# Kernel tuning notes

Hardware: AMD Instinct MI355X
Metric: run time of the kernel (lower is better)

Reference implementation:

```python
import jax, jax.numpy as jnp
import numpy as np

L, B, E, H, NL = 512, 8, 1024, 16, 2
HD = E // H
DFF = 4 * E
EPS = 1e-5


def setup_inputs() -> dict:
    key = jax.random.key(0)
    ks = jax.random.split(key, 8)
    s = 0.02
    return {
        "src": jax.random.normal(ks[0], (L, B, E), jnp.float32),
        "position_embed": jax.random.normal(ks[1], (L, L, HD), jnp.float32) * s,
        "type_embed": jax.random.normal(ks[2], (L, L, HD), jnp.float32) * s,
        "Wi": jax.random.normal(ks[3], (NL, 3 * E, E), jnp.float32) * s,
        "bi": jnp.zeros((NL, 3 * E), jnp.float32),
        "Wo": jax.random.normal(ks[4], (NL, E, E), jnp.float32) * s,
        "bo": jnp.zeros((NL, E), jnp.float32),
        "W1": jax.random.normal(ks[5], (NL, DFF, E), jnp.float32) * s,
        "b1": jnp.zeros((NL, DFF), jnp.float32),
        "W2": jax.random.normal(ks[6], (NL, E, DFF), jnp.float32) * s,
        "b2": jnp.zeros((NL, E), jnp.float32),
        "g1": jnp.ones((NL, E), jnp.float32),
        "be1": jnp.zeros((NL, E), jnp.float32),
        "g2": jnp.ones((NL, E), jnp.float32),
        "be2": jnp.zeros((NL, E), jnp.float32),
    }


def _ln(x, g, b):
    m = jnp.mean(x, -1, keepdims=True)
    v = jnp.mean((x - m) ** 2, -1, keepdims=True)
    return (x - m) * jax.lax.rsqrt(v + EPS) * g + b


def _attn(src, pos, typ, Wi, bi, Wo, bo):
    # src: [L, B, E]
    p = src @ Wi.T + bi                      # [L, B, 3E]
    q, k, v = jnp.split(p, 3, axis=-1)
    q = q * (HD ** -0.5)
    # -> [B, H, L, HD]
    def hsplit(t):
        return t.reshape(L, B, H, HD).transpose(1, 2, 0, 3)
    q, k, v = hsplit(q), hsplit(k), hsplit(v)
    # scores = q k^T + type_embed@q + q@pos^T  (Shaw relative attention)
    scores = jnp.einsum('bhld,bhsd->bhls', q, k)
    scores = scores + jnp.einsum('bhld,lsd->bhls', q, pos)      # position term
    scores = scores + jnp.einsum('lsd,bhld->bhls', typ, q)      # type term
    w = jax.nn.softmax(scores, axis=-1)                          # [B, H, L, S]
    # output = w v + w@pos + typ^T@w
    out = jnp.einsum('bhls,bhsd->bhld', w, v)
    out = out + jnp.einsum('bhls,lsd->bhld', w, pos)
    out = out + jnp.einsum('bhls,lsd->bhld', w, typ)
    out = out.transpose(2, 0, 1, 3).reshape(L, B, E)            # [L, B, E]
    return out @ Wo.T + bo


def _layer(src, pos, typ, Wi, bi, Wo, bo, W1, b1, W2, b2, g1, be1, g2, be2):
    src2 = _attn(src, pos, typ, Wi, bi, Wo, bo)
    src = _ln(src + src2, g1, be1)
    h = jax.nn.gelu(src @ W1.T + b1, approximate=False)
    src2 = h @ W2.T + b2
    return _ln(src + src2, g2, be2)


def reference(src, position_embed, type_embed, Wi, bi, Wo, bo, W1, b1, W2, b2,
              g1, be1, g2, be2):
    out = src
    for i in range(NL):
        out = _layer(out, position_embed, type_embed,
                     Wi[i], bi[i], Wo[i], bo[i], W1[i], b1[i], W2[i], b2[i],
                     g1[i], be1[i], g2[i], be2[i])
    return out
```

## Files before the change

kernel.cpp:

```cpp
#include <hip/hip_runtime.h>
#include <hip/hip_bf16.h>
#include <math.h>


typedef __hip_bfloat16 bf16;
typedef short short8 __attribute__((ext_vector_type(8)));
typedef float f32x4 __attribute__((ext_vector_type(4)));

constexpr int Lc = 512;
constexpr int Bc = 8;
constexpr int Ec = 1024;
constexpr int Hc = 16;
constexpr int HDc = 64;
constexpr int NLc = 2;
constexpr int DFFc = 4096;
constexpr int LB = Lc * Bc;
constexpr int BHc = Bc * Hc;
constexpr float EPSc = 1e-5f;

__device__ inline unsigned short f2bfu(float f) {
  union { __hip_bfloat16 h; unsigned short u; } cv;
  cv.h = __float2bfloat16(f);
  return cv.u;
}

template <bool ACC, bool GELU, bool OBF>
__global__ __launch_bounds__(256) void gemm_bt(
    int M, int N, int K,
    const bf16* __restrict__ A, int lda, long long sAz,
    const bf16* __restrict__ Bm, int ldb, long long sBz,
    void* __restrict__ Cv, int ldc, long long sCz,
    const float* __restrict__ bias) {
  __shared__ __align__(16) bf16 As[128 * 72];
  __shared__ __align__(16) bf16 Bs[64 * 72];
  const int tid = threadIdx.x;
  const int w = tid >> 6, lane = tid & 63, quad = lane >> 4, lr = lane & 15;
  const int m0 = blockIdx.x * 128, n0 = blockIdx.y * 64;
  const long long z = blockIdx.z;
  A += z * sAz;
  Bm += z * sBz;
  float* Cf = (float*)Cv;
  bf16* Cb = (bf16*)Cv;

  f32x4 acc[2][4];
#pragma unroll
  for (int i = 0; i < 2; i++)
#pragma unroll
    for (int j = 0; j < 4; j++) acc[i][j] = {0.f, 0.f, 0.f, 0.f};

  for (int k0 = 0; k0 < K; k0 += 64) {
#pragma unroll
    for (int i = 0; i < 8; i++) {
      int slot = tid + i * 256;
      int r = slot >> 4, c4 = (slot & 15) << 2;
      const bf16* srcp = A + (long long)(m0 + r) * lda + k0 + c4;
      *(ushort4*)&As[r * 72 + c4] = *(const ushort4*)srcp;
    }
#pragma unroll
    for (int i = 0; i < 4; i++) {
      int slot = tid + i * 256;
      int r = slot >> 4, c4 = (slot & 15) << 2;
      const bf16* srcp = Bm + (long long)(n0 + r) * ldb + k0 + c4;
      *(ushort4*)&Bs[r * 72 + c4] = *(const ushort4*)srcp;
    }
    __syncthreads();
#pragma unroll
    for (int ks = 0; ks < 64; ks += 32) {
      short8 a[2], b[4];
#pragma unroll
      for (int i = 0; i < 2; i++)
        a[i] = *(const short8*)&As[(w * 32 + i * 16 + lr) * 72 + ks + quad * 8];
#pragma unroll
      for (int j = 0; j < 4; j++)
        b[j] = *(const short8*)&Bs[(j * 16 + lr) * 72 + ks + quad * 8];
#pragma unroll
      for (int i = 0; i < 2; i++)
#pragma unroll
        for (int j = 0; j < 4; j++)
          acc[i][j] = __builtin_amdgcn_mfma_f32_16x16x32_bf16(a[i], b[j], acc[i][j], 0, 0, 0);
    }
    __syncthreads();
  }

#pragma unroll
  for (int i = 0; i < 2; i++) {
#pragma unroll
    for (int j = 0; j < 4; j++) {
      int col = n0 + j * 16 + lr;
      float bv = bias ? bias[col] : 0.f;
#pragma unroll
      for (int r = 0; r < 4; r++) {
        int row = m0 + w * 32 + i * 16 + quad * 4 + r;
        long long off = z * sCz + (long long)row * ldc + col;
        float v = acc[i][j][r] + bv;
        if (ACC) v += Cf[off];
        if (GELU) v = 0.5f * v * (1.f + erff(v * 0.70710678118654752f));
        if (OBF)
          Cb[off] = __float2bfloat16(v);
        else
          Cf[off] = v;
      }
    }
  }
}

__global__ void cvt_bf16(const float* __restrict__ in, bf16* __restrict__ out, long long n) {
  long long i = (long long)blockIdx.x * 256 + threadIdx.x;
  if (i < n) out[i] = __float2bfloat16(in[i]);
}

__global__ void init_x(const float* __restrict__ src, float* __restrict__ x, bf16* __restrict__ xb) {
  long long i = (long long)blockIdx.x * 256 + threadIdx.x;
  float v = src[i];
  x[i] = v;
  xb[i] = __float2bfloat16(v);
}

__global__ void prep_R(const float* __restrict__ pos, const float* __restrict__ typ,
                       bf16* __restrict__ Rb, bf16* __restrict__ Rt) {
  __shared__ __align__(16) float Ls[64 * 68];
  int l = blockIdx.y, s0 = blockIdx.x * 64;
  int tid = threadIdx.x;
#pragma unroll
  for (int i = 0; i < 4; i++) {
    int slot = tid + i * 256;
    int r = slot >> 4, c = (slot & 15) << 2;
    long long off = (((long long)l) * Lc + s0 + r) * HDc + c;
    float4 a = *(const float4*)&pos[off];
    float4 b = *(const float4*)&typ[off];
    float4 s = {a.x + b.x, a.y + b.y, a.z + b.z, a.w + b.w};
    *(float4*)&Ls[r * 68 + c] = s;
    ushort4 o = {f2bfu(s.x), f2bfu(s.y), f2bfu(s.z), f2bfu(s.w)};
    *(ushort4*)&Rb[off] = o;
  }
  __syncthreads();
#pragma unroll
  for (int i = 0; i < 4; i++) {
    int slot = tid + i * 256;
    int d = slot >> 4, s4 = (slot & 15) << 2;
    ushort4 o = {f2bfu(Ls[(s4 + 0) * 68 + d]), f2bfu(Ls[(s4 + 1) * 68 + d]),
                 f2bfu(Ls[(s4 + 2) * 68 + d]), f2bfu(Ls[(s4 + 3) * 68 + d])};
    *(ushort4*)&Rt[(((long long)l) * HDc + d) * Lc + s0 + s4] = o;
  }
}

__global__ void split_qk(const float* __restrict__ P, bf16* __restrict__ q, bf16* __restrict__ k) {
  long long idx = (long long)blockIdx.x * 256 + threadIdx.x;
  int col = idx & (Ec - 1);
  long long row = idx >> 10;
  int l = (int)(row >> 3), b = (int)(row & 7);
  int h = col >> 6, d = col & 63;
  long long dst = (((long long)(b * Hc + h)) * Lc + l) * HDc + d;
  q[dst] = __float2bfloat16(P[row * 3072 + col] * 0.125f);
  k[dst] = __float2bfloat16(P[row * 3072 + Ec + col]);
}

__global__ void transpose_v(const float* __restrict__ P, bf16* __restrict__ vt) {
  __shared__ __align__(16) float Ls[64 * 68];
  int bh = blockIdx.y, b = bh >> 4, h = bh & 15;
  int l0 = blockIdx.x * 64;
  int tid = threadIdx.x;
#pragma unroll
  for (int i = 0; i < 4; i++) {
    int slot = tid + i * 256;
    int r = slot >> 4, c = (slot & 15) << 2;
    float4 v = *(const float4*)&P[((long long)(l0 + r) * Bc + b) * 3072 + 2 * Ec + h * 64 + c];
    *(float4*)&Ls[r * 68 + c] = v;
  }
  __syncthreads();
#pragma unroll
  for (int i = 0; i < 4; i++) {
    int slot = tid + i * 256;
    int d = slot >> 4, s4 = (slot & 15) << 2;
    ushort4 o = {f2bfu(Ls[(s4 + 0) * 68 + d]), f2bfu(Ls[(s4 + 1) * 68 + d]),
                 f2bfu(Ls[(s4 + 2) * 68 + d]), f2bfu(Ls[(s4 + 3) * 68 + d])};
    *(ushort4*)&vt[(((long long)(b * Hc + h)) * HDc + d) * Lc + l0 + s4] = o;
  }
}

__global__ __launch_bounds__(256) void softmax_rows(const float* S, bf16* P) {
  int w = threadIdx.x >> 6, lane = threadIdx.x & 63;
  long long row = (long long)blockIdx.x * 4 + w;
  const float* sr = S + row * 512;
  float4 v0 = *(const float4*)(sr + lane * 4);
  float4 v1 = *(const float4*)(sr + 256 + lane * 4);
  float mx = fmaxf(fmaxf(fmaxf(v0.x, v0.y), fmaxf(v0.z, v0.w)),
                   fmaxf(fmaxf(v1.x, v1.y), fmaxf(v1.z, v1.w)));
#pragma unroll
  for (int o = 32; o; o >>= 1) mx = fmaxf(mx, __shfl_xor(mx, o, 64));
  float e[8];
  e[0] = __expf(v0.x - mx); e[1] = __expf(v0.y - mx);
  e[2] = __expf(v0.z - mx); e[3] = __expf(v0.w - mx);
  e[4] = __expf(v1.x - mx); e[5] = __expf(v1.y - mx);
  e[6] = __expf(v1.z - mx); e[7] = __expf(v1.w - mx);
  float sum = e[0] + e[1] + e[2] + e[3] + e[4] + e[5] + e[6] + e[7];
#pragma unroll
  for (int o = 32; o; o >>= 1) sum += __shfl_xor(sum, o, 64);
  float inv = 1.f / sum;
  ushort4 o0 = {f2bfu(e[0] * inv), f2bfu(e[1] * inv), f2bfu(e[2] * inv), f2bfu(e[3] * inv)};
  ushort4 o1 = {f2bfu(e[4] * inv), f2bfu(e[5] * inv), f2bfu(e[6] * inv), f2bfu(e[7] * inv)};
  *(ushort4*)(P + row * 1024 + lane * 4) = o0;
  *(ushort4*)(P + row * 1024 + 256 + lane * 4) = o1;
}

__global__ void merge_ao(const float* __restrict__ ao2, bf16* __restrict__ aob) {
  long long i = (long long)blockIdx.x * 256 + threadIdx.x;
  int d = (int)(i & 63);
  long long t = i >> 6;
  int l = (int)(t & (Lc - 1));
  long long bh = t >> 9;
  int b = (int)(bh >> 4), h = (int)(bh & 15);
  aob[((long long)(l * Bc + b)) * Ec + h * 64 + d] = __float2bfloat16(ao2[i]);
}

__global__ __launch_bounds__(256) void add_ln(const float* __restrict__ X, const float* __restrict__ Cin,
                                              const float* __restrict__ g, const float* __restrict__ be,
                                              float* __restrict__ outF, bf16* __restrict__ outB) {
  __shared__ float s_sum[4], s_sq[4];
  long long row = blockIdx.x;
  int tid = threadIdx.x;
  float4 xv = *(const float4*)&X[row * Ec + tid * 4];
  float4 cv = *(const float4*)&Cin[row * Ec + tid * 4];
  float v[4] = {xv.x + cv.x, xv.y + cv.y, xv.z + cv.z, xv.w + cv.w};
  float sm = v[0] + v[1] + v[2] + v[3];
  float sq = v[0] * v[0] + v[1] * v[1] + v[2] * v[2] + v[3] * v[3];
#pragma unroll
  for (int o = 32; o; o >>= 1) {
    sm += __shfl_xor(sm, o, 64);
    sq += __shfl_xor(sq, o, 64);
  }
  int w = tid >> 6, lane = tid & 63;
  if (lane == 0) {
    s_sum[w] = sm;
    s_sq[w] = sq;
  }
  __syncthreads();
  sm = s_sum[0] + s_sum[1] + s_sum[2] + s_sum[3];
  sq = s_sq[0] + s_sq[1] + s_sq[2] + s_sq[3];
  float mean = sm * (1.f / Ec);
  float var = sq * (1.f / Ec) - mean * mean;
  float rs = rsqrtf(var + EPSc);
#pragma unroll
  for (int e = 0; e < 4; e++) {
    int n = tid * 4 + e;
    float o = (v[e] - mean) * rs * g[n] + be[n];
    outF[row * Ec + n] = o;
    outB[row * Ec + n] = __float2bfloat16(o);
  }
}

static constexpr size_t WS_NEED = 327155712;

struct GlobalWs {
  void* p = nullptr;
  GlobalWs() {
    if (hipMalloc(&p, WS_NEED) != hipSuccess) p = nullptr;
  }
};
static GlobalWs g_ws;

extern "C" void kernel_launch(void* const* d_in, const int* in_sizes, int n_in,
                              void* d_out, int out_size, void* d_ws, size_t ws_size,
                              hipStream_t stream) {
  const float* src = (const float*)d_in[0];
  const float* pos = (const float*)d_in[1];
  const float* typ = (const float*)d_in[2];
  const float* Wi = (const float*)d_in[3];
  const float* bi = (const float*)d_in[4];
  const float* Wo = (const float*)d_in[5];
  const float* bo = (const float*)d_in[6];
  const float* W1 = (const float*)d_in[7];
  const float* b1 = (const float*)d_in[8];
  const float* W2 = (const float*)d_in[9];
  const float* b2 = (const float*)d_in[10];
  const float* g1 = (const float*)d_in[11];
  const float* be1 = (const float*)d_in[12];
  const float* g2 = (const float*)d_in[13];
  const float* be2 = (const float*)d_in[14];
  float* out = (float*)d_out;
  (void)in_sizes; (void)n_in; (void)out_size;

  char* wp = (ws_size >= WS_NEED) ? (char*)d_ws : (char*)g_ws.p;
  if (!wp) wp = (char*)d_ws;
  auto alloc = [&](size_t bytes) {
    char* r = wp;
    wp += (bytes + 255) & ~(size_t)255;
    return r;
  };

  char* U = alloc((size_t)BHc * Lc * Lc * 4);
  float* P = (float*)U;
  float* scores = (float*)U;
  bf16* probs = (bf16*)U;
  bf16* hb = (bf16*)U;

  float* x = (float*)alloc((size_t)LB * Ec * 4);
  bf16* xb = (bf16*)alloc((size_t)LB * Ec * 2);
  bf16* q = (bf16*)alloc((size_t)BHc * Lc * HDc * 2);
  bf16* k = (bf16*)alloc((size_t)BHc * Lc * HDc * 2);
  bf16* vt = (bf16*)alloc((size_t)BHc * HDc * Lc * 2);
  float* ao2 = (float*)alloc((size_t)BHc * Lc * HDc * 4);
  float* c1 = ao2;
  bf16* aob = (bf16*)alloc((size_t)LB * Ec * 2);
  bf16* Rb = (bf16*)alloc((size_t)Lc * Lc * HDc * 2);
  bf16* Rt = (bf16*)alloc((size_t)Lc * HDc * Lc * 2);
  bf16* wib = (bf16*)alloc((size_t)NLc * 3 * Ec * Ec * 2);
  bf16* wob = (bf16*)alloc((size_t)NLc * Ec * Ec * 2);
  bf16* w1b = (bf16*)alloc((size_t)NLc * DFFc * Ec * 2);
  bf16* w2b = (bf16*)alloc((size_t)NLc * Ec * DFFc * 2);

  {
    long long n;
    n = (long long)NLc * 3 * Ec * Ec;
    cvt_bf16<<<(int)((n + 255) / 256), 256, 0, stream>>>(Wi, wib, n);
    n = (long long)NLc * Ec * Ec;
    cvt_bf16<<<(int)((n + 255) / 256), 256, 0, stream>>>(Wo, wob, n);
    n = (long long)NLc * DFFc * Ec;
    cvt_bf16<<<(int)((n + 255) / 256), 256, 0, stream>>>(W1, w1b, n);
    n = (long long)NLc * Ec * DFFc;
    cvt_bf16<<<(int)((n + 255) / 256), 256, 0, stream>>>(W2, w2b, n);
  }
  prep_R<<<dim3(Lc / 64, Lc), 256, 0, stream>>>(pos, typ, Rb, Rt);
  init_x<<<LB * Ec / 256, 256, 0, stream>>>(src, x, xb);

  for (int i = 0; i < NLc; i++) {
    const bf16* Wi_b = wib + (size_t)i * 3 * Ec * Ec;
    const bf16* Wo_b = wob + (size_t)i * Ec * Ec;
    const bf16* W1_b = w1b + (size_t)i * DFFc * Ec;
    const bf16* W2_b = w2b + (size_t)i * Ec * DFFc;

    gemm_bt<false, false, false><<<dim3(LB / 128, 3 * Ec / 64, 1), 256, 0, stream>>>(
        LB, 3 * Ec, Ec, xb, Ec, 0, Wi_b, Ec, 0, P, 3 * Ec, 0, bi + (size_t)i * 3 * Ec);
    split_qk<<<LB * Ec / 256, 256, 0, stream>>>(P, q, k);
    transpose_v<<<dim3(Lc / 64, BHc), 256, 0, stream>>>(P, vt);

    gemm_bt<false, false, false><<<dim3(Lc / 128, Lc / 64, BHc), 256, 0, stream>>>(
        Lc, Lc, HDc, q, HDc, (long long)Lc * HDc, k, HDc, (long long)Lc * HDc,
        scores, Lc, (long long)Lc * Lc, nullptr);
    gemm_bt<true, false, false><<<dim3(1, Lc / 64, Lc), 256, 0, stream>>>(
        BHc, Lc, HDc, q, Lc * HDc, (long long)HDc, Rb, HDc, (long long)Lc * HDc,
        scores, Lc * Lc, (long long)Lc, nullptr);

    softmax_rows<<<BHc * Lc / 4, 256, 0, stream>>>(scores, probs);

    gemm_bt<false, false, false><<<dim3(Lc / 128, 1, BHc), 256, 0, stream>>>(
        Lc, HDc, Lc, probs, 1024, (long long)Lc * 1024, vt, Lc, (long long)HDc * Lc,
        ao2, HDc, (long long)Lc * HDc, nullptr);
    gemm_bt<true, false, false><<<dim3(1, 1, Lc), 256, 0, stream>>>(
        BHc, HDc, Lc, probs, Lc * 1024, (long long)1024, Rt, Lc, (long long)HDc * Lc,
        ao2, Lc * HDc, (long long)HDc, nullptr);

    merge_ao<<<BHc * Lc * HDc / 256, 256, 0, stream>>>(ao2, aob);

    gemm_bt<false, false, false><<<dim3(LB / 128, Ec / 64, 1), 256, 0, stream>>>(
        LB, Ec, Ec, aob, Ec, 0, Wo_b, Ec, 0, c1, Ec, 0, bo + (size_t)i * Ec);
    add_ln<<<LB, 256, 0, stream>>>(x, c1, g1 + (size_t)i * Ec, be1 + (size_t)i * Ec, x, xb);

    gemm_bt<false, true, true><<<dim3(LB / 128, DFFc / 64, 1), 256, 0, stream>>>(
        LB, DFFc, Ec, xb, Ec, 0, W1_b, Ec, 0, hb, DFFc, 0, b1 + (size_t)i * DFFc);
    gemm_bt<false, false, false><<<dim3(LB / 128, Ec / 64, 1), 256, 0, stream>>>(
        LB, Ec, DFFc, hb, DFFc, 0, W2_b, DFFc, 0, c1, Ec, 0, b2 + (size_t)i * Ec);

    float* outF = (i == NLc - 1) ? out : x;
    add_ln<<<LB, 256, 0, stream>>>(x, c1, g2 + (size_t)i * Ec, be2 + (size_t)i * Ec, outF, xb);
  }
}
```

Baseline: 1.221 ms.

## Add 128x128 GEMM with direct-to-LDS async loads and XOR swizzle

Adds a new GEMM kernel with a 128x128 output tile (4x4 MFMA tiles per wave in a 2x2 wave grid) that loads A/B tiles via global_load_lds directly into LDS using an XOR-swizzled layout instead of padded rows. The projection, FFN and QK/position-score GEMMs now use it, doubling reuse per loaded tile and avoiding register staging and padding. It uses more accumulator registers and halves the block count in the N dimension, which may reduce occupancy. The kernel has no double buffering, so loads still serialize with compute.

```diff
diff --git a/kernel.cpp b/kernel.cpp
--- a/kernel.cpp
+++ b/kernel.cpp
@@ -22,6 +22,100 @@
   union { __hip_bfloat16 h; unsigned short u; } cv;
   cv.h = __float2bfloat16(f);
   return cv.u;
+}
+
+__device__ inline void async16(const bf16* gsrc, bf16* ldst) {
+  __builtin_amdgcn_global_load_lds(
+      (const __attribute__((address_space(1))) void*)gsrc,
+      (__attribute__((address_space(3))) void*)ldst, 16, 0, 0);
+}
+
+template <bool ACC, bool GELU, bool OBF>
+__global__ __launch_bounds__(256) void gemm128(
+    int M, int N, int K,
+    const bf16* __restrict__ A, long long lda, long long sAz,
+    const bf16* __restrict__ Bm, long long ldb, long long sBz,
+    void* __restrict__ Cv, long long ldc, long long sCz,
+    const float* __restrict__ bias) {
+  __shared__ __align__(16) bf16 As[128 * 64];
+  __shared__ __align__(16) bf16 Bs[128 * 64];
+  const int tid = threadIdx.x;
+  const int w = tid >> 6, lane = tid & 63, quad = lane >> 4, lr = lane & 15;
+  const int wm = w >> 1, wn = w & 1;
+  const int m0 = blockIdx.x * 128, n0 = blockIdx.y * 128;
+  const long long z = blockIdx.z;
+  const bf16* Az = A + z * sAz;
+  const bf16* Bz = Bm + z * sBz;
+  float* Cf = (float*)Cv;
+  bf16* Cb = (bf16*)Cv;
+
+  const int srow = lane >> 3, sj = lane & 7;
+  const int sc = sj ^ srow;
+
+  f32x4 acc[4][4];
+#pragma unroll
+  for (int i = 0; i < 4; i++)
+#pragma unroll
+    for (int j = 0; j < 4; j++) acc[i][j] = {0.f, 0.f, 0.f, 0.f};
+
+  for (int k0 = 0; k0 < K; k0 += 64) {
+#pragma unroll
+    for (int s = 0; s < 4; s++) {
+      int li = w * 4 + s;
+      int r = li * 8 + srow;
+      async16(Az + (long long)(m0 + r) * lda + k0 + sc * 8, &As[li * 512]);
+    }
+#pragma unroll
+    for (int s = 0; s < 4; s++) {
+      int li = w * 4 + s;
+      int r = li * 8 + srow;
+      async16(Bz + (long long)(n0 + r) * ldb + k0 + sc * 8, &Bs[li * 512]);
+    }
+    __syncthreads();
+#pragma unroll
+    for (int ks = 0; ks < 64; ks += 32) {
+      const int gc = (ks >> 3) + quad;
+      const int jc = gc ^ (lr & 7);
+      short8 a[4], b[4];
+#pragma unroll
+      for (int i = 0; i < 4; i++) {
+        int row = wm * 64 + i * 16 + lr;
+        a[i] = *(const short8*)&As[row * 64 + jc * 8];
+      }
+#pragma unroll
+      for (int j = 0; j < 4; j++) {
+        int row = wn * 64 + j * 16 + lr;
+        b[j] = *(const short8*)&Bs[row * 64 + jc * 8];
+      }
+#pragma unroll
+      for (int i = 0; i < 4; i++)
+#pragma unroll
+        for (int j = 0; j < 4; j++)
+          acc[i][j] = __builtin_amdgcn_mfma_f32_16x16x32_bf16(a[i], b[j], acc[i][j], 0, 0, 0);
+    }
+    __syncthreads();
+  }
+
+#pragma unroll
+  for (int j = 0; j < 4; j++) {
+    int col = n0 + wn * 64 + j * 16 + lr;
+    float bv = bias ? bias[col] : 0.f;
+#pragma unroll
+    for (int i = 0; i < 4; i++) {
+#pragma unroll
+      for (int r = 0; r < 4; r++) {
+        int row = m0 + wm * 64 + i * 16 + quad * 4 + r;
+        long long off = z * sCz + (long long)row * ldc + col;
+        float v = acc[i][j][r] + bv;
+        if (ACC) v += Cf[off];
+        if (GELU) v = 0.5f * v * (1.f + erff(v * 0.70710678118654752f));
+        if (OBF)
+          Cb[off] = __float2bfloat16(v);
+        else
+          Cf[off] = v;
+      }
+    }
+  }
 }
 
 template <bool ACC, bool GELU, bool OBF>
@@ -53,15 +147,13 @@
     for (int i = 0; i < 8; i++) {
       int slot = tid + i * 256;
       int r = slot >> 4, c4 = (slot & 15) << 2;
-      const bf16* srcp = A + (long long)(m0 + r) * lda + k0 + c4;
-      *(ushort4*)&As[r * 72 + c4] = *(const ushort4*)srcp;
+      *(ushort4*)&As[r * 72 + c4] = *(const ushort4*)(A + (long long)(m0 + r) * lda + k0 + c4);
     }
 #pragma unroll
     for (int i = 0; i < 4; i++) {
       int slot = tid + i * 256;
       int r = slot >> 4, c4 = (slot & 15) << 2;
-      const bf16* srcp = Bm + (long long)(n0 + r) * ldb + k0 + c4;
-      *(ushort4*)&Bs[r * 72 + c4] = *(const ushort4*)srcp;
+      *(ushort4*)&Bs[r * 72 + c4] = *(const ushort4*)(Bm + (long long)(n0 + r) * ldb + k0 + c4);
     }
     __syncthreads();
 #pragma unroll
@@ -329,17 +421,17 @@
     const bf16* W1_b = w1b + (size_t)i * DFFc * Ec;
     const bf16* W2_b = w2b + (size_t)i * Ec * DFFc;
 
-    gemm_bt<false, false, false><<<dim3(LB / 128, 3 * Ec / 64, 1), 256, 0, stream>>>(
+    gemm128<false, false, false><<<dim3(LB / 128, 3 * Ec / 128, 1), 256, 0, stream>>>(
         LB, 3 * Ec, Ec, xb, Ec, 0, Wi_b, Ec, 0, P, 3 * Ec, 0, bi + (size_t)i * 3 * Ec);
     split_qk<<<LB * Ec / 256, 256, 0, stream>>>(P, q, k);
     transpose_v<<<dim3(Lc / 64, BHc), 256, 0, stream>>>(P, vt);
 
-    gemm_bt<false, false, false><<<dim3(Lc / 128, Lc / 64, BHc), 256, 0, stream>>>(
+    gemm128<false, false, false><<<dim3(Lc / 128, Lc / 128, BHc), 256, 0, stream>>>(
         Lc, Lc, HDc, q, HDc, (long long)Lc * HDc, k, HDc, (long long)Lc * HDc,
         scores, Lc, (long long)Lc * Lc, nullptr);
-    gemm_bt<true, false, false><<<dim3(1, Lc / 64, Lc), 256, 0, stream>>>(
-        BHc, Lc, HDc, q, Lc * HDc, (long long)HDc, Rb, HDc, (long long)Lc * HDc,
-        scores, Lc * Lc, (long long)Lc, nullptr);
+    gemm128<true, false, false><<<dim3(1, Lc / 128, Lc), 256, 0, stream>>>(
+        BHc, Lc, HDc, q, (long long)Lc * HDc, (long long)HDc, Rb, HDc, (long long)Lc * HDc,
+        scores, (long long)Lc * Lc, (long long)Lc, nullptr);
 
     softmax_rows<<<BHc * Lc / 4, 256, 0, stream>>>(scores, probs);
 
@@ -352,13 +444,13 @@
 
     merge_ao<<<BHc * Lc * HDc / 256, 256, 0, stream>>>(ao2, aob);
 
-    gemm_bt<false, false, false><<<dim3(LB / 128, Ec / 64, 1), 256, 0, stream>>>(
+    gemm128<false, false, false><<<dim3(LB / 128, Ec / 128, 1), 256, 0, stream>>>(
         LB, Ec, Ec, aob, Ec, 0, Wo_b, Ec, 0, c1, Ec, 0, bo + (size_t)i * Ec);
     add_ln<<<LB, 256, 0, stream>>>(x, c1, g1 + (size_t)i * Ec, be1 + (size_t)i * Ec, x, xb);
 
-    gemm_bt<false, true, true><<<dim3(LB / 128, DFFc / 64, 1), 256, 0, stream>>>(
+    gemm128<false, true, true><<<dim3(LB / 128, DFFc / 128, 1), 256, 0, stream>>>(
         LB, DFFc, Ec, xb, Ec, 0, W1_b, Ec, 0, hb, DFFc, 0, b1 + (size_t)i * DFFc);
-    gemm_bt<false, false, false><<<dim3(LB / 128, Ec / 64, 1), 256, 0, stream>>>(
+    gemm128<false, false, false><<<dim3(LB / 128, Ec / 128, 1), 256, 0, stream>>>(
         LB, Ec, DFFc, hb, DFFc, 0, W2_b, DFFc, 0, c1, Ec, 0, b2 + (size_t)i * Ec);
 
     float* outF = (i == NLc - 1) ? out : x;
```

Result: no change. 1.241 ms (+1.6%).
